# Optimization experiments

Measured on AMD Instinct MI355X. Metric: run time of the kernel, lower is better.

The kernel has to match this reference:

```python
import jax, jax.numpy as jnp
import numpy as np
import itertools

N_SUBSETS = 4
TAU = 0.1


def setup_inputs() -> dict:
    key = jax.random.key(0)
    k1, k2, k3 = jax.random.split(key, 3)
    # scale projections so exp(sim/tau) stays numerically sane (module assumes small/normalized projections)
    projections = jax.random.normal(k1, (8192, 128), dtype=jnp.float32) * 0.05
    xrecon = jax.random.normal(k2, (8192, 784), dtype=jnp.float32)
    recon_label = jax.random.normal(k3, (8192, 784), dtype=jnp.float32)
    return {"projections": projections, "xrecon": xrecon, "recon_label": recon_label}


def _joint_loss(projections, xrecon, recon_label):
    # reconstruction MSE
    recon_loss = jnp.mean(jnp.square(xrecon - recon_label))

    # ---- XNegloss (SimCLR-style with n_subsets positives per group) ----
    N, D = projections.shape
    sim = (projections @ projections.T) / TAU  # [N, N] dot similarity
    gid = jnp.arange(N) // N_SUBSETS
    pos_mask = gid[:, None] == gid[None, :]  # same-group entries are positives
    exp_sim = jnp.exp(sim)
    # original code drops positive entries exactly equal to 1 (positives[positives != 1])
    pos_sum = jnp.sum(jnp.where(pos_mask & (sim != 1.0), exp_sim, 0.0), axis=-1)
    neg_sum = jnp.sum(jnp.where(pos_mask, 0.0, exp_sim), axis=-1)
    closs = jnp.mean(-jnp.log(pos_sum / (pos_sum + neg_sum)))

    # ---- distance loss: MSE over all subset pairs within each group ----
    combi = np.array(list(itertools.combinations(range(N_SUBSETS), 2)))
    left, right = combi[:, 0], combi[:, 1]
    P = projections.reshape(N // N_SUBSETS, N_SUBSETS, D)
    # per-group mean over (pairs, D) then mean over groups == global mean (equal counts)
    dist_loss = jnp.mean(jnp.square(P[:, left] - P[:, right]))

    loss = recon_loss + closs + dist_loss
    return loss, closs, recon_loss, dist_loss


def reference(projections, xrecon, recon_label):
    return _joint_loss(projections, xrecon, recon_label)
```

## Files before the change

### kernel.cpp

```cpp
#include <hip/hip_runtime.h>
#include <hip/hip_bf16.h>
#include <stdint.h>

typedef __bf16 bf16x8 __attribute__((ext_vector_type(8)));
typedef float  f32x4  __attribute__((ext_vector_type(4)));

#define NROWS   8192
#define DIMK    128
#define NGROUPS 2048
#define RECON_N 6422528
#define RECON_BLOCKS 1568
#define GROUP_BLOCKS 512
#define CONV_BLOCKS  1024
#define PREP_BLOCKS (RECON_BLOCKS + GROUP_BLOCKS + CONV_BLOCKS)
#define SIM_BLOCKS   1024

#define WS_S      0
#define WS_G      8192
#define WS_E      16384
#define WS_RPART  24576
#define WS_DPART  26144
#define WS_PB     26656

__device__ __forceinline__ void async16(const void* g, void* l) {
    __builtin_amdgcn_global_load_lds(
        (const __attribute__((address_space(1))) void*)g,
        (__attribute__((address_space(3))) void*)l, 16, 0, 0);
}

__device__ __forceinline__ unsigned short f2bf(float f) {
    union { __hip_bfloat16 h; unsigned short u; } v;
    v.h = __float2bfloat16(f);
    return v.u;
}

__global__ __launch_bounds__(256) void prep_kernel(
        const float* __restrict__ Pf,
        const float4* __restrict__ X,
        const float4* __restrict__ Y,
        uint2* __restrict__ Pb,
        float* __restrict__ ws) {
    const int bx = blockIdx.x;
    const int wave = threadIdx.x >> 6, lane = threadIdx.x & 63;

    if (bx < RECON_BLOCKS) {
        __shared__ float red[4];
        int base = bx * 1024 + threadIdx.x;
        float4 a0 = X[base],       b0 = Y[base];
        float4 a1 = X[base + 256], b1 = Y[base + 256];
        float4 a2 = X[base + 512], b2 = Y[base + 512];
        float4 a3 = X[base + 768], b3 = Y[base + 768];
        float s = 0.f, d;
        d = a0.x - b0.x; s += d * d;  d = a0.y - b0.y; s += d * d;
        d = a0.z - b0.z; s += d * d;  d = a0.w - b0.w; s += d * d;
        d = a1.x - b1.x; s += d * d;  d = a1.y - b1.y; s += d * d;
        d = a1.z - b1.z; s += d * d;  d = a1.w - b1.w; s += d * d;
        d = a2.x - b2.x; s += d * d;  d = a2.y - b2.y; s += d * d;
        d = a2.z - b2.z; s += d * d;  d = a2.w - b2.w; s += d * d;
        d = a3.x - b3.x; s += d * d;  d = a3.y - b3.y; s += d * d;
        d = a3.z - b3.z; s += d * d;  d = a3.w - b3.w; s += d * d;
#pragma unroll
        for (int mm = 1; mm < 64; mm <<= 1) s += __shfl_xor(s, mm, 64);
        if (lane == 0) red[wave] = s;
        __syncthreads();
        if (threadIdx.x == 0)
            ws[WS_RPART + bx] = red[0] + red[1] + red[2] + red[3];
    } else if (bx < RECON_BLOCKS + GROUP_BLOCKS) {
        __shared__ float dred[4];
        int gb = bx - RECON_BLOCKS;
        float* G = ws + WS_G;
        float* E = ws + WS_E;
        int g = gb * 4 + wave;
        const float* base = Pf + (size_t)g * 4 * DIMK;
        float v[4][2];
#pragma unroll
        for (int r = 0; r < 4; ++r) {
            v[r][0] = base[r * DIMK + lane];
            v[r][1] = base[r * DIMK + 64 + lane];
        }
        float dmat[4][4];
#pragma unroll
        for (int r = 0; r < 4; ++r)
#pragma unroll
            for (int s2 = r; s2 < 4; ++s2) {
                float p = v[r][0] * v[s2][0] + v[r][1] * v[s2][1];
#pragma unroll
                for (int mm = 1; mm < 64; mm <<= 1) p += __shfl_xor(p, mm, 64);
                dmat[r][s2] = p; dmat[s2][r] = p;
            }
        if (lane == 0) {
            float distp = 0.f;
#pragma unroll
            for (int r = 0; r < 4; ++r)
#pragma unroll
                for (int s2 = r + 1; s2 < 4; ++s2)
                    distp += dmat[r][r] + dmat[s2][s2] - 2.f * dmat[r][s2];
            dred[wave] = distp;
#pragma unroll
            for (int r = 0; r < 4; ++r) {
                float Gs = 0.f, Es = 0.f;
#pragma unroll
                for (int s2 = 0; s2 < 4; ++s2) {
                    float sim = dmat[r][s2] * 10.0f;
                    float e = __expf(sim);
                    Gs += e;
                    if (sim == 1.0f) Es += e;
                }
                G[g * 4 + r] = Gs;
                E[g * 4 + r] = Es;
            }
        }
        __syncthreads();
        if (threadIdx.x == 0)
            ws[WS_DPART + gb] = dred[0] + dred[1] + dred[2] + dred[3];
    } else {
        int cb = bx - (RECON_BLOCKS + GROUP_BLOCKS);
        int idx = cb * 256 + threadIdx.x;
        float4 a = ((const float4*)Pf)[idx];
        uint2 r;
        r.x = (uint32_t)f2bf(a.x) | ((uint32_t)f2bf(a.y) << 16);
        r.y = (uint32_t)f2bf(a.z) | ((uint32_t)f2bf(a.w) << 16);
        Pb[idx] = r;
    }
}

__global__ __launch_bounds__(256, 3) void sim_kernel(
        const unsigned short* __restrict__ Pb,
        float* __restrict__ S) {
    __shared__ unsigned short tile[128 * 128];
    const int bx = blockIdx.x;
    const int wave = threadIdx.x >> 6, lane = threadIdx.x & 63;
    const int wr = wave >> 1, wc = wave & 1;
    const int rowBase = (bx >> 4) * 128;
    const int colBase = (bx & 15) * 512;
    const int m = lane & 15, kq = lane >> 4;

    int srcOff[8];
#pragma unroll
    for (int i = 0; i < 8; ++i) {
        int seg = i * 4 + wave;
        int chunk = seg * 64 + lane;
        int r = chunk >> 4, qp = chunk & 15;
        int q = (qp - r) & 15;
        srcOff[i] = r * 256 + q * 16;
    }

    {
        const char* g = (const char*)(Pb + (size_t)rowBase * DIMK);
#pragma unroll
        for (int i = 0; i < 8; ++i) {
            int seg = i * 4 + wave;
            async16(g + srcOff[i], (char*)tile + seg * 1024 + lane * 16);
        }
    }
    __syncthreads();

    bf16x8 Af[4][4];
#pragma unroll
    for (int i = 0; i < 4; ++i) {
        int rl = wr * 64 + i * 16 + m;
#pragma unroll
        for (int kk = 0; kk < 4; ++kk)
            Af[i][kk] = *(const bf16x8*)((const char*)tile + rl * 256 +
                                         (((kq + kk * 4 + rl) & 15) << 4));
    }
    __syncthreads();

    float rowAcc[4][4];
#pragma unroll
    for (int i = 0; i < 4; ++i)
#pragma unroll
        for (int r = 0; r < 4; ++r) rowAcc[i][r] = 0.f;

    for (int t = 0; t < 4; ++t) {
        {
            const char* g = (const char*)(Pb + (size_t)(colBase + t * 128) * DIMK);
#pragma unroll
            for (int i = 0; i < 8; ++i) {
                int seg = i * 4 + wave;
                async16(g + srcOff[i], (char*)tile + seg * 1024 + lane * 16);
            }
        }
        __syncthreads();

        f32x4 acc[4][4];
#pragma unroll
        for (int i = 0; i < 4; ++i)
#pragma unroll
            for (int j = 0; j < 4; ++j) acc[i][j] = (f32x4){0.f, 0.f, 0.f, 0.f};

#pragma unroll
        for (int kk = 0; kk < 4; ++kk) {
            bf16x8 Bf[4];
#pragma unroll
            for (int j = 0; j < 4; ++j) {
                int rl = wc * 64 + j * 16 + m;
                Bf[j] = *(const bf16x8*)((const char*)tile + rl * 256 +
                                         (((kq + kk * 4 + rl) & 15) << 4));
            }
#pragma unroll
            for (int i = 0; i < 4; ++i)
#pragma unroll
                for (int j = 0; j < 4; ++j)
                    acc[i][j] = __builtin_amdgcn_mfma_f32_16x16x32_bf16(
                        Af[i][kk], Bf[j], acc[i][j], 0, 0, 0);
        }
#pragma unroll
        for (int i = 0; i < 4; ++i)
#pragma unroll
            for (int j = 0; j < 4; ++j)
#pragma unroll
                for (int r = 0; r < 4; ++r)
                    rowAcc[i][r] += __expf(acc[i][j][r] * 10.0f);
        __syncthreads();
    }

#pragma unroll
    for (int i = 0; i < 4; ++i)
#pragma unroll
        for (int r = 0; r < 4; ++r) {
            float sv = rowAcc[i][r];
            sv += __shfl_xor(sv, 1, 64);
            sv += __shfl_xor(sv, 2, 64);
            sv += __shfl_xor(sv, 4, 64);
            sv += __shfl_xor(sv, 8, 64);
            rowAcc[i][r] = sv;
        }
    if ((lane & 15) == 0) {
        int c = lane >> 4;
#pragma unroll
        for (int i = 0; i < 4; ++i)
#pragma unroll
            for (int r = 0; r < 4; ++r)
                atomicAdd(&S[rowBase + wr * 64 + i * 16 + c * 4 + r], rowAcc[i][r]);
    }
}

__global__ __launch_bounds__(1024) void finalize_kernel(const float* __restrict__ ws,
                                                        float* __restrict__ out) {
    __shared__ float redc[16], redr[16], redd[16];
    const float* S = ws + WS_S;
    const float* G = ws + WS_G;
    const float* E = ws + WS_E;

    float c = 0.f;
    for (int r = threadIdx.x; r < NROWS; r += 1024)
        c += __logf(S[r] - E[r]) - __logf(G[r] - E[r]);
    float rs = 0.f;
    for (int i = threadIdx.x; i < RECON_BLOCKS; i += 1024) rs += ws[WS_RPART + i];
    float ds = 0.f;
    for (int i = threadIdx.x; i < GROUP_BLOCKS; i += 1024) ds += ws[WS_DPART + i];

#pragma unroll
    for (int mm = 1; mm < 64; mm <<= 1) {
        c  += __shfl_xor(c,  mm, 64);
        rs += __shfl_xor(rs, mm, 64);
        ds += __shfl_xor(ds, mm, 64);
    }
    int wave = threadIdx.x >> 6, lane = threadIdx.x & 63;
    if (lane == 0) { redc[wave] = c; redr[wave] = rs; redd[wave] = ds; }
    __syncthreads();
    if (threadIdx.x == 0) {
        float cs = 0.f, rss = 0.f, dss = 0.f;
#pragma unroll
        for (int i = 0; i < 16; ++i) { cs += redc[i]; rss += redr[i]; dss += redd[i]; }
        float closs = cs / (float)NROWS;
        float recon = rss / (float)RECON_N;
        float dist  = dss / (float)(NGROUPS * 6 * DIMK);
        out[0] = recon + closs + dist;
        out[1] = closs;
        out[2] = recon;
        out[3] = dist;
    }
}

extern "C" void kernel_launch(void* const* d_in, const int* in_sizes, int n_in,
                              void* d_out, int out_size, void* d_ws, size_t ws_size,
                              hipStream_t stream) {
    const float* P  = (const float*)d_in[0];
    const float4* X = (const float4*)d_in[1];
    const float4* Y = (const float4*)d_in[2];
    float* out = (float*)d_out;
    float* w = (float*)d_ws;
    unsigned short* Pb = (unsigned short*)(w + WS_PB);

    hipMemsetAsync(w + WS_S, 0, NROWS * sizeof(float), stream);
    prep_kernel<<<PREP_BLOCKS, 256, 0, stream>>>(P, X, Y, (uint2*)Pb, w);
    sim_kernel<<<SIM_BLOCKS, 256, 0, stream>>>(Pb, w + WS_S);
    finalize_kernel<<<1, 1024, 0, stream>>>(w, out);
}
```

Before: 138.0 us.

## Fuse sim, recon, group work and finalize into one interleaved mega kernel

Restructures the pipeline: the memset is folded into a small prep kernel that converts projections to bf16. The similarity tiles are interleaved with the memory-bound recon MSE and group blocks in one mega kernel, so compute and bandwidth work overlap. The last block to finish, found through an atomic counter, does the finalize reduction. This removes two launches and the memset, and the A fragments are now loaded directly from global memory. The cost is threadfence and atomic overhead, plus the LDS footprint that the recon blocks now carry.

```diff
diff --git a/kernel.cpp b/kernel.cpp
--- a/kernel.cpp
+++ b/kernel.cpp
@@ -9,18 +9,19 @@
 #define DIMK    128
 #define NGROUPS 2048
 #define RECON_N 6422528
+#define SIM_BLOCKS   1024
 #define RECON_BLOCKS 1568
 #define GROUP_BLOCKS 512
-#define CONV_BLOCKS  1024
-#define PREP_BLOCKS (RECON_BLOCKS + GROUP_BLOCKS + CONV_BLOCKS)
-#define SIM_BLOCKS   1024
+#define MEGA_BLOCKS  3104
+#define PREP_BLOCKS  1032
 
 #define WS_S      0
 #define WS_G      8192
 #define WS_E      16384
 #define WS_RPART  24576
 #define WS_DPART  26144
-#define WS_PB     26656
+#define WS_DONE   26656
+#define WS_PB     26672
 
 __device__ __forceinline__ void async16(const void* g, void* l) {
     __builtin_amdgcn_global_load_lds(
@@ -34,18 +35,138 @@
     return v.u;
 }
 
-__global__ __launch_bounds__(256) void prep_kernel(
+__global__ __launch_bounds__(256) void prep_kernel(const float4* __restrict__ Pf,
+                                                   uint2* __restrict__ Pb,
+                                                   float* __restrict__ ws) {
+    int bx = blockIdx.x;
+    if (bx < 1024) {
+        int idx = bx * 256 + threadIdx.x;
+        float4 a = Pf[idx];
+        uint2 r;
+        r.x = (uint32_t)f2bf(a.x) | ((uint32_t)f2bf(a.y) << 16);
+        r.y = (uint32_t)f2bf(a.z) | ((uint32_t)f2bf(a.w) << 16);
+        Pb[idx] = r;
+    } else {
+        int zb = bx - 1024;
+        ((float4*)(ws + WS_S))[zb * 256 + threadIdx.x] = (float4){0.f, 0.f, 0.f, 0.f};
+        if (zb == 0 && threadIdx.x == 0)
+            *(int*)(ws + WS_DONE) = 0;
+    }
+}
+
+__global__ __launch_bounds__(256, 3) void mega_kernel(
+        const unsigned short* __restrict__ Pb,
         const float* __restrict__ Pf,
         const float4* __restrict__ X,
         const float4* __restrict__ Y,
-        uint2* __restrict__ Pb,
-        float* __restrict__ ws) {
+        float* __restrict__ ws,
+        float* __restrict__ out) {
+    __shared__ unsigned short tile[128 * 128];
+    __shared__ int isLast;
     const int bx = blockIdx.x;
     const int wave = threadIdx.x >> 6, lane = threadIdx.x & 63;
 
-    if (bx < RECON_BLOCKS) {
+    int role, idx;
+    if (bx < 3072) {
+        int r6 = bx % 6, c6 = bx / 6;
+        if (r6 == 0)      { role = 0; idx = c6 * 2; }
+        else if (r6 == 3) { role = 0; idx = c6 * 2 + 1; }
+        else if (r6 == 5) { role = 2; idx = c6; }
+        else              { role = 1; idx = c6 * 3 + (r6 == 1 ? 0 : (r6 == 2 ? 1 : 2)); }
+    } else {
+        role = 1; idx = 1536 + (bx - 3072);
+    }
+
+    if (role == 0) {
+        float* S = ws + WS_S;
+        const int wr = wave >> 1, wc = wave & 1;
+        const int rowBase = (idx >> 4) * 128;
+        const int colBase = (idx & 15) * 512;
+        const int m = lane & 15, kq = lane >> 4;
+
+        bf16x8 Af[4][4];
+#pragma unroll
+        for (int i = 0; i < 4; ++i) {
+            const unsigned short* rowp =
+                Pb + (size_t)(rowBase + wr * 64 + i * 16 + m) * DIMK + kq * 8;
+#pragma unroll
+            for (int kk = 0; kk < 4; ++kk)
+                Af[i][kk] = *(const bf16x8*)(rowp + kk * 32);
+        }
+
+        int srcOff[8];
+#pragma unroll
+        for (int i = 0; i < 8; ++i) {
+            int chunk = (i * 4 + wave) * 64 + lane;
+            int r = chunk >> 4, qp = chunk & 15;
+            srcOff[i] = r * 256 + (((qp - r) & 15) << 4);
+        }
+
+        float rowAcc[4][4];
+#pragma unroll
+        for (int i = 0; i < 4; ++i)
+#pragma unroll
+            for (int r = 0; r < 4; ++r) rowAcc[i][r] = 0.f;
+
+        for (int t = 0; t < 4; ++t) {
+            {
+                const char* g = (const char*)(Pb + (size_t)(colBase + t * 128) * DIMK);
+#pragma unroll
+                for (int i = 0; i < 8; ++i) {
+                    int seg = i * 4 + wave;
+                    async16(g + srcOff[i], (char*)tile + seg * 1024 + lane * 16);
+                }
+            }
+            __syncthreads();
+
+#pragma unroll
+            for (int j = 0; j < 4; ++j) {
+                int rl = wc * 64 + j * 16 + m;
+                bf16x8 Bf[4];
+#pragma unroll
+                for (int kk = 0; kk < 4; ++kk)
+                    Bf[kk] = *(const bf16x8*)((const char*)tile + rl * 256 +
+                                              (((kq + kk * 4 + rl) & 15) << 4));
+                f32x4 acc[4];
+#pragma unroll
+                for (int i = 0; i < 4; ++i) acc[i] = (f32x4){0.f, 0.f, 0.f, 0.f};
+#pragma unroll
+                for (int kk = 0; kk < 4; ++kk)
+#pragma unroll
+                    for (int i = 0; i < 4; ++i)
+                        acc[i] = __builtin_amdgcn_mfma_f32_16x16x32_bf16(
+                            Af[i][kk], Bf[kk], acc[i], 0, 0, 0);
+#pragma unroll
+                for (int i = 0; i < 4; ++i)
+#pragma unroll
+                    for (int r = 0; r < 4; ++r)
+                        rowAcc[i][r] += __expf(acc[i][r] * 10.0f);
+            }
+            __syncthreads();
+        }
+
+#pragma unroll
+        for (int i = 0; i < 4; ++i)
+#pragma unroll
+            for (int r = 0; r < 4; ++r) {
+                float sv = rowAcc[i][r];
+                sv += __shfl_xor(sv, 1, 64);
+                sv += __shfl_xor(sv, 2, 64);
+                sv += __shfl_xor(sv, 4, 64);
+                sv += __shfl_xor(sv, 8, 64);
+                rowAcc[i][r] = sv;
+            }
+        if ((lane & 15) == 0) {
+            int c = lane >> 4;
+#pragma unroll
+            for (int i = 0; i < 4; ++i)
+#pragma unroll
+                for (int r = 0; r < 4; ++r)
+                    atomicAdd(&S[rowBase + wr * 64 + i * 16 + c * 4 + r], rowAcc[i][r]);
+        }
+    } else if (role == 1) {
         __shared__ float red[4];
-        int base = bx * 1024 + threadIdx.x;
+        int base = idx * 1024 + threadIdx.x;
         float4 a0 = X[base],       b0 = Y[base];
         float4 a1 = X[base + 256], b1 = Y[base + 256];
         float4 a2 = X[base + 512], b2 = Y[base + 512];
@@ -64,13 +185,12 @@
         if (lane == 0) red[wave] = s;
         __syncthreads();
         if (threadIdx.x == 0)
-            ws[WS_RPART + bx] = red[0] + red[1] + red[2] + red[3];
-    } else if (bx < RECON_BLOCKS + GROUP_BLOCKS) {
+            ws[WS_RPART + idx] = red[0] + red[1] + red[2] + red[3];
+    } else {
         __shared__ float dred[4];
-        int gb = bx - RECON_BLOCKS;
         float* G = ws + WS_G;
         float* E = ws + WS_E;
-        int g = gb * 4 + wave;
+        int g = idx * 4 + wave;
         const float* base = Pf + (size_t)g * 4 * DIMK;
         float v[4][2];
 #pragma unroll
@@ -112,165 +232,46 @@
         }
         __syncthreads();
         if (threadIdx.x == 0)
-            ws[WS_DPART + gb] = dred[0] + dred[1] + dred[2] + dred[3];
-    } else {
-        int cb = bx - (RECON_BLOCKS + GROUP_BLOCKS);
-        int idx = cb * 256 + threadIdx.x;
-        float4 a = ((const float4*)Pf)[idx];
-        uint2 r;
-        r.x = (uint32_t)f2bf(a.x) | ((uint32_t)f2bf(a.y) << 16);
-        r.y = (uint32_t)f2bf(a.z) | ((uint32_t)f2bf(a.w) << 16);
-        Pb[idx] = r;
-    }
-}
-
-__global__ __launch_bounds__(256, 3) void sim_kernel(
-        const unsigned short* __restrict__ Pb,
-        float* __restrict__ S) {
-    __shared__ unsigned short tile[128 * 128];
-    const int bx = blockIdx.x;
-    const int wave = threadIdx.x >> 6, lane = threadIdx.x & 63;
-    const int wr = wave >> 1, wc = wave & 1;
-    const int rowBase = (bx >> 4) * 128;
-    const int colBase = (bx & 15) * 512;
-    const int m = lane & 15, kq = lane >> 4;
-
-    int srcOff[8];
-#pragma unroll
-    for (int i = 0; i < 8; ++i) {
-        int seg = i * 4 + wave;
-        int chunk = seg * 64 + lane;
-        int r = chunk >> 4, qp = chunk & 15;
-        int q = (qp - r) & 15;
-        srcOff[i] = r * 256 + q * 16;
-    }
-
-    {
-        const char* g = (const char*)(Pb + (size_t)rowBase * DIMK);
-#pragma unroll
-        for (int i = 0; i < 8; ++i) {
-            int seg = i * 4 + wave;
-            async16(g + srcOff[i], (char*)tile + seg * 1024 + lane * 16);
-        }
-    }
-    __syncthreads();
-
-    bf16x8 Af[4][4];
-#pragma unroll
-    for (int i = 0; i < 4; ++i) {
-        int rl = wr * 64 + i * 16 + m;
-#pragma unroll
-        for (int kk = 0; kk < 4; ++kk)
-            Af[i][kk] = *(const bf16x8*)((const char*)tile + rl * 256 +
-                                         (((kq + kk * 4 + rl) & 15) << 4));
-    }
-    __syncthreads();
-
-    float rowAcc[4][4];
-#pragma unroll
-    for (int i = 0; i < 4; ++i)
-#pragma unroll
-        for (int r = 0; r < 4; ++r) rowAcc[i][r] = 0.f;
-
-    for (int t = 0; t < 4; ++t) {
-        {
-            const char* g = (const char*)(Pb + (size_t)(colBase + t * 128) * DIMK);
-#pragma unroll
-            for (int i = 0; i < 8; ++i) {
-                int seg = i * 4 + wave;
-                async16(g + srcOff[i], (char*)tile + seg * 1024 + lane * 16);
-            }
-        }
-        __syncthreads();
-
-        f32x4 acc[4][4];
-#pragma unroll
-        for (int i = 0; i < 4; ++i)
-#pragma unroll
-            for (int j = 0; j < 4; ++j) acc[i][j] = (f32x4){0.f, 0.f, 0.f, 0.f};
-
-#pragma unroll
-        for (int kk = 0; kk < 4; ++kk) {
-            bf16x8 Bf[4];
-#pragma unroll
-            for (int j = 0; j < 4; ++j) {
-                int rl = wc * 64 + j * 16 + m;
-                Bf[j] = *(const bf16x8*)((const char*)tile + rl * 256 +
-                                         (((kq + kk * 4 + rl) & 15) << 4));
-            }
-#pragma unroll
-            for (int i = 0; i < 4; ++i)
-#pragma unroll
-                for (int j = 0; j < 4; ++j)
-                    acc[i][j] = __builtin_amdgcn_mfma_f32_16x16x32_bf16(
-                        Af[i][kk], Bf[j], acc[i][j], 0, 0, 0);
-        }
-#pragma unroll
-        for (int i = 0; i < 4; ++i)
-#pragma unroll
-            for (int j = 0; j < 4; ++j)
-#pragma unroll
-                for (int r = 0; r < 4; ++r)
-                    rowAcc[i][r] += __expf(acc[i][j][r] * 10.0f);
-        __syncthreads();
-    }
-
-#pragma unroll
-    for (int i = 0; i < 4; ++i)
-#pragma unroll
-        for (int r = 0; r < 4; ++r) {
-            float sv = rowAcc[i][r];
-            sv += __shfl_xor(sv, 1, 64);
-            sv += __shfl_xor(sv, 2, 64);
-            sv += __shfl_xor(sv, 4, 64);
-            sv += __shfl_xor(sv, 8, 64);
-            rowAcc[i][r] = sv;
-        }
-    if ((lane & 15) == 0) {
-        int c = lane >> 4;
-#pragma unroll
-        for (int i = 0; i < 4; ++i)
-#pragma unroll
-            for (int r = 0; r < 4; ++r)
-                atomicAdd(&S[rowBase + wr * 64 + i * 16 + c * 4 + r], rowAcc[i][r]);
-    }
-}
-
-__global__ __launch_bounds__(1024) void finalize_kernel(const float* __restrict__ ws,
-                                                        float* __restrict__ out) {
-    __shared__ float redc[16], redr[16], redd[16];
-    const float* S = ws + WS_S;
-    const float* G = ws + WS_G;
-    const float* E = ws + WS_E;
-
-    float c = 0.f;
-    for (int r = threadIdx.x; r < NROWS; r += 1024)
-        c += __logf(S[r] - E[r]) - __logf(G[r] - E[r]);
-    float rs = 0.f;
-    for (int i = threadIdx.x; i < RECON_BLOCKS; i += 1024) rs += ws[WS_RPART + i];
-    float ds = 0.f;
-    for (int i = threadIdx.x; i < GROUP_BLOCKS; i += 1024) ds += ws[WS_DPART + i];
-
-#pragma unroll
-    for (int mm = 1; mm < 64; mm <<= 1) {
-        c  += __shfl_xor(c,  mm, 64);
-        rs += __shfl_xor(rs, mm, 64);
-        ds += __shfl_xor(ds, mm, 64);
-    }
-    int wave = threadIdx.x >> 6, lane = threadIdx.x & 63;
-    if (lane == 0) { redc[wave] = c; redr[wave] = rs; redd[wave] = ds; }
+            ws[WS_DPART + idx] = dred[0] + dred[1] + dred[2] + dred[3];
+    }
+
+    __threadfence();
     __syncthreads();
     if (threadIdx.x == 0) {
-        float cs = 0.f, rss = 0.f, dss = 0.f;
-#pragma unroll
-        for (int i = 0; i < 16; ++i) { cs += redc[i]; rss += redr[i]; dss += redd[i]; }
-        float closs = cs / (float)NROWS;
-        float recon = rss / (float)RECON_N;
-        float dist  = dss / (float)(NGROUPS * 6 * DIMK);
-        out[0] = recon + closs + dist;
-        out[1] = closs;
-        out[2] = recon;
-        out[3] = dist;
+        int old = atomicAdd((int*)(ws + WS_DONE), 1);
+        isLast = (old == MEGA_BLOCKS - 1);
+    }
+    __syncthreads();
+    if (isLast) {
+        __threadfence();
+        __shared__ float redc[4], redr[4], redd[4];
+        const float* S = ws + WS_S;
+        const float* G = ws + WS_G;
+        const float* E = ws + WS_E;
+        float c = 0.f;
+        for (int r = threadIdx.x; r < NROWS; r += 256)
+            c += __logf(S[r] - E[r]) - __logf(G[r] - E[r]);
+        float rs = 0.f;
+        for (int i = threadIdx.x; i < RECON_BLOCKS; i += 256) rs += ws[WS_RPART + i];
+        float ds = 0.f;
+        for (int i = threadIdx.x; i < GROUP_BLOCKS; i += 256) ds += ws[WS_DPART + i];
+#pragma unroll
+        for (int mm = 1; mm < 64; mm <<= 1) {
+            c  += __shfl_xor(c,  mm, 64);
+            rs += __shfl_xor(rs, mm, 64);
+            ds += __shfl_xor(ds, mm, 64);
+        }
+        if (lane == 0) { redc[wave] = c; redr[wave] = rs; redd[wave] = ds; }
+        __syncthreads();
+        if (threadIdx.x == 0) {
+            float closs = (redc[0] + redc[1] + redc[2] + redc[3]) / (float)NROWS;
+            float recon = (redr[0] + redr[1] + redr[2] + redr[3]) / (float)RECON_N;
+            float dist  = (redd[0] + redd[1] + redd[2] + redd[3]) / (float)(NGROUPS * 6 * DIMK);
+            out[0] = recon + closs + dist;
+            out[1] = closs;
+            out[2] = recon;
+            out[3] = dist;
+        }
     }
 }
 
@@ -284,8 +285,6 @@
     float* w = (float*)d_ws;
     unsigned short* Pb = (unsigned short*)(w + WS_PB);
 
-    hipMemsetAsync(w + WS_S, 0, NROWS * sizeof(float), stream);
-    prep_kernel<<<PREP_BLOCKS, 256, 0, stream>>>(P, X, Y, (uint2*)Pb, w);
-    sim_kernel<<<SIM_BLOCKS, 256, 0, stream>>>(Pb, w + WS_S);
-    finalize_kernel<<<1, 1024, 0, stream>>>(w, out);
-}
+    prep_kernel<<<PREP_BLOCKS, 256, 0, stream>>>((const float4*)P, (uint2*)Pb, w);
+    mega_kernel<<<MEGA_BLOCKS, 256, 0, stream>>>(Pb, P, X, Y, w, out);
+}
```

Result: slower. 431.3 us (+212.6%).
